# Optimization experiments

Hardware: AMD Instinct MI355X
Metric: run time of the kernel (lower is better)

Reference implementation:

```python
import jax, jax.numpy as jnp
import numpy as np


def setup_inputs() -> dict:
    key = jax.random.key(0)
    z = jax.random.normal(key, (8, 4096, 1024), dtype=jnp.float32)
    return {"z": z}


def reference(z):
    d = z.shape[-1]
    # sort descending along last dim
    z_sorted = -jnp.sort(-z, axis=-1)
    z_cumsum = jnp.cumsum(z_sorted, axis=-1)
    k = jnp.arange(1, d + 1, dtype=z.dtype)  # [d]
    rhs = 1 + k * z_sorted
    is_gt = (rhs > z_cumsum).astype(z.dtype)
    # largest k satisfying the support condition
    k_z = jnp.max(is_gt * k, axis=-1, keepdims=True)  # [..., 1]
    idx = k_z.astype(jnp.int32) - 1
    z_cumsum_k = jnp.take_along_axis(z_cumsum, idx, axis=-1)
    tau = (z_cumsum_k - 1) / k_z
    p = jnp.clip(z - tau, 0.0, None)
    return p
```

## Files before the change

### kernel.cpp

```cpp
#include <hip/hip_runtime.h>


#define ROW_D 1024

typedef float f4 __attribute__((ext_vector_type(4)));

template <int CTRL, int RMASK>
__device__ __forceinline__ float dpp_mv(float x) {
    return __builtin_bit_cast(float, __builtin_amdgcn_update_dpp(
        __builtin_bit_cast(int, x), __builtin_bit_cast(int, x),
        CTRL, RMASK, 0xf, false));
}

__device__ __forceinline__ float dpp_sum_to63(float x) {
    x += dpp_mv<0x111, 0xf>(x);
    x += dpp_mv<0x112, 0xf>(x);
    x += dpp_mv<0x114, 0xf>(x);
    x += dpp_mv<0x118, 0xf>(x);
    x += dpp_mv<0x142, 0xa>(x);
    x += dpp_mv<0x143, 0xc>(x);
    return x;
}
__device__ __forceinline__ float dpp_max_to63(float x) {
    x = fmaxf(x, dpp_mv<0x111, 0xf>(x));
    x = fmaxf(x, dpp_mv<0x112, 0xf>(x));
    x = fmaxf(x, dpp_mv<0x114, 0xf>(x));
    x = fmaxf(x, dpp_mv<0x118, 0xf>(x));
    x = fmaxf(x, dpp_mv<0x142, 0xa>(x));
    x = fmaxf(x, dpp_mv<0x143, 0xc>(x));
    return x;
}
__device__ __forceinline__ float bcast63(float x) {
    return __builtin_bit_cast(float,
        __builtin_amdgcn_readlane(__builtin_bit_cast(int, x), 63));
}

__global__ __launch_bounds__(256) void sparsemax_kernel(
    const float* __restrict__ z, float* __restrict__ out, int nrows) {
    const int lane = (int)(threadIdx.x & 63u);
    const int row  = (int)(blockIdx.x << 2) + (int)(threadIdx.x >> 6);
    if (row >= nrows) return;

    const f4* __restrict__ zin = reinterpret_cast<const f4*>(z + (size_t)row * ROW_D);
    f4* __restrict__ pout      = reinterpret_cast<f4*>(out + (size_t)row * ROW_D);

    f4 v[4];
#pragma unroll
    for (int j = 0; j < 4; ++j) v[j] = zin[lane + 64 * j];

    float mj[4];
#pragma unroll
    for (int j = 0; j < 4; ++j)
        mj[j] = fmaxf(fmaxf(v[j].x, v[j].y), fmaxf(v[j].z, v[j].w));
    float m = fmaxf(fmaxf(mj[0], mj[1]), fmaxf(mj[2], mj[3]));
    m = bcast63(dpp_max_to63(m));

    float t = m - 1.0f;
#pragma unroll 1
    for (int it = 0; it < 16; ++it) {
        float sj[4];
        int n = 0;
#pragma unroll
        for (int j = 0; j < 4; ++j) {
            const float d0 = v[j].x - t, d1 = v[j].y - t;
            const float d2 = v[j].z - t, d3 = v[j].w - t;
            sj[j] = (fmaxf(d0, 0.0f) + fmaxf(d1, 0.0f)) +
                    (fmaxf(d2, 0.0f) + fmaxf(d3, 0.0f));
            n += __popcll(__ballot(d0 > 0.0f));
            n += __popcll(__ballot(d1 > 0.0f));
            n += __popcll(__ballot(d2 > 0.0f));
            n += __popcll(__ballot(d3 > 0.0f));
        }
        float S = bcast63(dpp_sum_to63((sj[0] + sj[1]) + (sj[2] + sj[3])));
        const float t2 = t + (S - 1.0f) / (float)n;
        if (t2 - t <= 1e-6f) { t = t2; break; }
        t = t2;
    }

#pragma unroll
    for (int j = 0; j < 4; ++j) {
        f4 o;
        o.x = fmaxf(v[j].x - t, 0.0f);
        o.y = fmaxf(v[j].y - t, 0.0f);
        o.z = fmaxf(v[j].z - t, 0.0f);
        o.w = fmaxf(v[j].w - t, 0.0f);
        __builtin_nontemporal_store(o, pout + lane + 64 * j);
    }
}

extern "C" void kernel_launch(void* const* d_in, const int* in_sizes, int n_in,
                              void* d_out, int out_size, void* d_ws, size_t ws_size,
                              hipStream_t stream) {
    const float* z = (const float*)d_in[0];
    float* out = (float*)d_out;
    const int n = in_sizes[0];
    const int nrows = n / ROW_D;
    const int blocks = (nrows + 3) / 4;
    sparsemax_kernel<<<blocks, 256, 0, stream>>>(z, out, nrows);
}
```

Measured before the change: 228.5 us.

## Use persistent grid-stride rows with double-buffered row prefetch and fast reciprocal

The kernel becomes persistent: the grid is capped at 2048 blocks and each wave walks rows with a grid stride. While it solves and stores the current row, it prefetches the next row into a second register buffer so load latency overlaps compute. The per-iteration division is replaced by v_rcp_f32, and the loop now exits on the step size. The extra buffer doubles the row registers per lane, which puts pressure on the 8-blocks occupancy hint.

```diff
diff --git a/kernel.cpp b/kernel.cpp
--- a/kernel.cpp
+++ b/kernel.cpp
@@ -34,20 +34,21 @@
     return __builtin_bit_cast(float,
         __builtin_amdgcn_readlane(__builtin_bit_cast(int, x), 63));
 }
+__device__ __forceinline__ float fast_rcp(float x) {
+    float r;
+    asm("v_rcp_f32 %0, %1" : "=v"(r) : "v"(x));
+    return r;
+}
 
-__global__ __launch_bounds__(256) void sparsemax_kernel(
-    const float* __restrict__ z, float* __restrict__ out, int nrows) {
-    const int lane = (int)(threadIdx.x & 63u);
-    const int row  = (int)(blockIdx.x << 2) + (int)(threadIdx.x >> 6);
-    if (row >= nrows) return;
+__device__ __forceinline__ void load_row(f4 (&v)[4], const float* __restrict__ z,
+                                         int row, int lane) {
+    const f4* __restrict__ p = reinterpret_cast<const f4*>(z + (size_t)row * ROW_D);
+#pragma unroll
+    for (int j = 0; j < 4; ++j) v[j] = p[lane + 64 * j];
+}
 
-    const f4* __restrict__ zin = reinterpret_cast<const f4*>(z + (size_t)row * ROW_D);
-    f4* __restrict__ pout      = reinterpret_cast<f4*>(out + (size_t)row * ROW_D);
-
-    f4 v[4];
-#pragma unroll
-    for (int j = 0; j < 4; ++j) v[j] = zin[lane + 64 * j];
-
+__device__ __forceinline__ void solve_store(f4 (&v)[4], float* __restrict__ out,
+                                            int row, int lane) {
     float mj[4];
 #pragma unroll
     for (int j = 0; j < 4; ++j)
@@ -71,12 +72,13 @@
             n += __popcll(__ballot(d2 > 0.0f));
             n += __popcll(__ballot(d3 > 0.0f));
         }
-        float S = bcast63(dpp_sum_to63((sj[0] + sj[1]) + (sj[2] + sj[3])));
-        const float t2 = t + (S - 1.0f) / (float)n;
-        if (t2 - t <= 1e-6f) { t = t2; break; }
-        t = t2;
+        const float S = bcast63(dpp_sum_to63((sj[0] + sj[1]) + (sj[2] + sj[3])));
+        const float step = (S - 1.0f) * fast_rcp((float)n);
+        t += step;
+        if (step <= 1e-6f) break;
     }
 
+    f4* __restrict__ p = reinterpret_cast<f4*>(out + (size_t)row * ROW_D);
 #pragma unroll
     for (int j = 0; j < 4; ++j) {
         f4 o;
@@ -84,7 +86,29 @@
         o.y = fmaxf(v[j].y - t, 0.0f);
         o.z = fmaxf(v[j].z - t, 0.0f);
         o.w = fmaxf(v[j].w - t, 0.0f);
-        __builtin_nontemporal_store(o, pout + lane + 64 * j);
+        __builtin_nontemporal_store(o, p + lane + 64 * j);
+    }
+}
+
+__global__ __launch_bounds__(256, 8) void sparsemax_kernel(
+    const float* __restrict__ z, float* __restrict__ out, int nrows) {
+    const int lane = (int)(threadIdx.x & 63u);
+    int r = (int)(blockIdx.x << 2) + (int)(threadIdx.x >> 6);
+    const int W = (int)(gridDim.x << 2);
+    if (r >= nrows) return;
+
+    f4 A[4], B[4];
+    load_row(A, z, r, lane);
+    int rn = r + W;
+    for (;;) {
+        if (rn < nrows) load_row(B, z, rn, lane);
+        solve_store(A, out, r, lane);
+        if (rn >= nrows) break;
+        r = rn + W;
+        if (r < nrows) load_row(A, z, r, lane);
+        solve_store(B, out, rn, lane);
+        if (r >= nrows) break;
+        rn = r + W;
     }
 }
 
@@ -95,6 +119,8 @@
     float* out = (float*)d_out;
     const int n = in_sizes[0];
     const int nrows = n / ROW_D;
-    const int blocks = (nrows + 3) / 4;
+    int blocks = 2048;
+    const int max_blocks = (nrows + 3) >> 2;
+    if (blocks > max_blocks) blocks = max_blocks;
     sparsemax_kernel<<<blocks, 256, 0, stream>>>(z, out, nrows);
 }
```

Measured after the change: 231.4 us. No clear change (+1.3%).

## Split sparsemax into tau-computation and elementwise apply kernels, use fast reciprocal

Applied to the files above, without the earlier changes.

When workspace is available, the fused kernel is split in two. The first kernel computes the per-row threshold tau and writes it to workspace; a second grid-stride kernel rereads z and writes the clipped output. The Newton step now uses a hardware v_rcp instead of a division, and the fused fallback drops the nontemporal store. The split reads the 128MB input twice to decouple the iterative reduction from the store stream, at the cost of an extra launch and more memory traffic.

```diff
diff --git a/kernel.cpp b/kernel.cpp
--- a/kernel.cpp
+++ b/kernel.cpp
@@ -34,16 +34,19 @@
     return __builtin_bit_cast(float,
         __builtin_amdgcn_readlane(__builtin_bit_cast(int, x), 63));
 }
+__device__ __forceinline__ float fast_rcp(float x) {
+    float r;
+    asm("v_rcp_f32 %0, %1" : "=v"(r) : "v"(x));
+    return r;
+}
 
-__global__ __launch_bounds__(256) void sparsemax_kernel(
-    const float* __restrict__ z, float* __restrict__ out, int nrows) {
+__global__ __launch_bounds__(256) void tau_kernel(
+    const float* __restrict__ z, float* __restrict__ tau, int nrows) {
     const int lane = (int)(threadIdx.x & 63u);
     const int row  = (int)(blockIdx.x << 2) + (int)(threadIdx.x >> 6);
     if (row >= nrows) return;
 
     const f4* __restrict__ zin = reinterpret_cast<const f4*>(z + (size_t)row * ROW_D);
-    f4* __restrict__ pout      = reinterpret_cast<f4*>(out + (size_t)row * ROW_D);
-
     f4 v[4];
 #pragma unroll
     for (int j = 0; j < 4; ++j) v[j] = zin[lane + 64 * j];
@@ -71,12 +74,70 @@
             n += __popcll(__ballot(d2 > 0.0f));
             n += __popcll(__ballot(d3 > 0.0f));
         }
-        float S = bcast63(dpp_sum_to63((sj[0] + sj[1]) + (sj[2] + sj[3])));
-        const float t2 = t + (S - 1.0f) / (float)n;
-        if (t2 - t <= 1e-6f) { t = t2; break; }
-        t = t2;
+        const float S = bcast63(dpp_sum_to63((sj[0] + sj[1]) + (sj[2] + sj[3])));
+        const float step = (S - 1.0f) * fast_rcp((float)n);
+        t += step;
+        if (step <= 1e-6f) break;
     }
+    if (lane == 0) tau[row] = t;
+}
 
+__global__ __launch_bounds__(256) void apply_kernel(
+    const float* __restrict__ z, const float* __restrict__ tau,
+    float* __restrict__ out, int n4) {
+    int i = (int)(blockIdx.x * blockDim.x + threadIdx.x);
+    const int stride = (int)(gridDim.x * blockDim.x);
+    const f4* __restrict__ zi = reinterpret_cast<const f4*>(z);
+    f4* __restrict__ po = reinterpret_cast<f4*>(out);
+    for (; i < n4; i += stride) {
+        const f4 v = zi[i];
+        const float t = tau[i >> 8];
+        f4 o;
+        o.x = fmaxf(v.x - t, 0.0f);
+        o.y = fmaxf(v.y - t, 0.0f);
+        o.z = fmaxf(v.z - t, 0.0f);
+        o.w = fmaxf(v.w - t, 0.0f);
+        po[i] = o;
+    }
+}
+
+__global__ __launch_bounds__(256) void sparsemax_fused(
+    const float* __restrict__ z, float* __restrict__ out, int nrows) {
+    const int lane = (int)(threadIdx.x & 63u);
+    const int row  = (int)(blockIdx.x << 2) + (int)(threadIdx.x >> 6);
+    if (row >= nrows) return;
+    const f4* __restrict__ zin = reinterpret_cast<const f4*>(z + (size_t)row * ROW_D);
+    f4* __restrict__ pout      = reinterpret_cast<f4*>(out + (size_t)row * ROW_D);
+    f4 v[4];
+#pragma unroll
+    for (int j = 0; j < 4; ++j) v[j] = zin[lane + 64 * j];
+    float mj[4];
+#pragma unroll
+    for (int j = 0; j < 4; ++j)
+        mj[j] = fmaxf(fmaxf(v[j].x, v[j].y), fmaxf(v[j].z, v[j].w));
+    float m = fmaxf(fmaxf(mj[0], mj[1]), fmaxf(mj[2], mj[3]));
+    m = bcast63(dpp_max_to63(m));
+    float t = m - 1.0f;
+#pragma unroll 1
+    for (int it = 0; it < 16; ++it) {
+        float sj[4];
+        int n = 0;
+#pragma unroll
+        for (int j = 0; j < 4; ++j) {
+            const float d0 = v[j].x - t, d1 = v[j].y - t;
+            const float d2 = v[j].z - t, d3 = v[j].w - t;
+            sj[j] = (fmaxf(d0, 0.0f) + fmaxf(d1, 0.0f)) +
+                    (fmaxf(d2, 0.0f) + fmaxf(d3, 0.0f));
+            n += __popcll(__ballot(d0 > 0.0f));
+            n += __popcll(__ballot(d1 > 0.0f));
+            n += __popcll(__ballot(d2 > 0.0f));
+            n += __popcll(__ballot(d3 > 0.0f));
+        }
+        const float S = bcast63(dpp_sum_to63((sj[0] + sj[1]) + (sj[2] + sj[3])));
+        const float step = (S - 1.0f) * fast_rcp((float)n);
+        t += step;
+        if (step <= 1e-6f) break;
+    }
 #pragma unroll
     for (int j = 0; j < 4; ++j) {
         f4 o;
@@ -84,7 +145,7 @@
         o.y = fmaxf(v[j].y - t, 0.0f);
         o.z = fmaxf(v[j].z - t, 0.0f);
         o.w = fmaxf(v[j].w - t, 0.0f);
-        __builtin_nontemporal_store(o, pout + lane + 64 * j);
+        pout[lane + 64 * j] = o;
     }
 }
 
@@ -95,6 +156,15 @@
     float* out = (float*)d_out;
     const int n = in_sizes[0];
     const int nrows = n / ROW_D;
-    const int blocks = (nrows + 3) / 4;
-    sparsemax_kernel<<<blocks, 256, 0, stream>>>(z, out, nrows);
+
+    if (d_ws != nullptr && ws_size >= (size_t)nrows * sizeof(float)) {
+        float* tau = (float*)d_ws;
+        const int blocks1 = (nrows + 3) / 4;
+        tau_kernel<<<blocks1, 256, 0, stream>>>(z, tau, nrows);
+        const int n4 = n / 4;
+        apply_kernel<<<2048, 256, 0, stream>>>(z, tau, out, n4);
+    } else {
+        const int blocks = (nrows + 3) / 4;
+        sparsemax_fused<<<blocks, 256, 0, stream>>>(z, out, nrows);
+    }
 }
```

Result: slower. 242.0 us (+5.9%).

## Iterate sparsemax threshold over per-lane top-4 candidates instead of all elements

Applied to the files above, without the earlier changes.

Each lane sorts its 16 values with a small sorting network and keeps the top 4. The Newton iteration for tau then runs only over those candidates whenever no lane's 4th-largest exceeds the starting threshold, with a fallback to the full 16-element loop otherwise. The division is replaced by a hardware reciprocal, and the output store is now a plain store instead of a nontemporal one. This adds sorting-network work up front to cut the per-iteration ALU and ballot cost, at some risk of precision differences from the approximate reciprocal.

```diff
diff --git a/kernel.cpp b/kernel.cpp
--- a/kernel.cpp
+++ b/kernel.cpp
@@ -34,6 +34,34 @@
     return __builtin_bit_cast(float,
         __builtin_amdgcn_readlane(__builtin_bit_cast(int, x), 63));
 }
+__device__ __forceinline__ float fast_rcp(float x) {
+    float r;
+    asm("v_rcp_f32 %0, %1" : "=v"(r) : "v"(x));
+    return r;
+}
+
+__device__ __forceinline__ void ce(float& a, float& b) {
+    const float hi = fmaxf(a, b);
+    const float lo = fminf(a, b);
+    a = hi; b = lo;
+}
+__device__ __forceinline__ void sort4(float& a, float& b, float& c, float& d) {
+    ce(a, b); ce(c, d); ce(a, c); ce(b, d); ce(b, c);
+}
+__device__ __forceinline__ void merge44_top4(
+    float A0, float A1, float A2, float A3,
+    float B0, float B1, float B2, float B3,
+    float& R0, float& R1, float& R2, float& R3) {
+    float e0 = A0, e1 = A2, e2 = B0, e3 = B2;
+    ce(e0, e2); ce(e1, e3); ce(e1, e2);
+    float o0 = A1, o1 = A3, o2 = B1, o3 = B3;
+    ce(o0, o2); ce(o1, o3); ce(o1, o2);
+    R0 = e0;
+    float x = o0, y = e1;
+    ce(x, y);
+    R1 = x; R2 = y;
+    R3 = fmaxf(o1, e2);
+}
 
 __global__ __launch_bounds__(256) void sparsemax_kernel(
     const float* __restrict__ z, float* __restrict__ out, int nrows) {
@@ -48,33 +76,59 @@
 #pragma unroll
     for (int j = 0; j < 4; ++j) v[j] = zin[lane + 64 * j];
 
-    float mj[4];
+    float g[4][4];
 #pragma unroll
-    for (int j = 0; j < 4; ++j)
-        mj[j] = fmaxf(fmaxf(v[j].x, v[j].y), fmaxf(v[j].z, v[j].w));
-    float m = fmaxf(fmaxf(mj[0], mj[1]), fmaxf(mj[2], mj[3]));
-    m = bcast63(dpp_max_to63(m));
+    for (int j = 0; j < 4; ++j) {
+        g[j][0] = v[j].x; g[j][1] = v[j].y; g[j][2] = v[j].z; g[j][3] = v[j].w;
+        sort4(g[j][0], g[j][1], g[j][2], g[j][3]);
+    }
+    float a0, a1, a2, a3, b0, b1, b2, b3, T0, T1, T2, T3;
+    merge44_top4(g[0][0], g[0][1], g[0][2], g[0][3],
+                 g[1][0], g[1][1], g[1][2], g[1][3], a0, a1, a2, a3);
+    merge44_top4(g[2][0], g[2][1], g[2][2], g[2][3],
+                 g[3][0], g[3][1], g[3][2], g[3][3], b0, b1, b2, b3);
+    merge44_top4(a0, a1, a2, a3, b0, b1, b2, b3, T0, T1, T2, T3);
 
+    const float m = bcast63(dpp_max_to63(T0));
     float t = m - 1.0f;
+
+    const unsigned long long bad = __ballot(T3 > t);
+    if (bad == 0ull) {
 #pragma unroll 1
-    for (int it = 0; it < 16; ++it) {
-        float sj[4];
-        int n = 0;
-#pragma unroll
-        for (int j = 0; j < 4; ++j) {
-            const float d0 = v[j].x - t, d1 = v[j].y - t;
-            const float d2 = v[j].z - t, d3 = v[j].w - t;
-            sj[j] = (fmaxf(d0, 0.0f) + fmaxf(d1, 0.0f)) +
-                    (fmaxf(d2, 0.0f) + fmaxf(d3, 0.0f));
-            n += __popcll(__ballot(d0 > 0.0f));
+        for (int it = 0; it < 16; ++it) {
+            const float d0 = T0 - t, d1 = T1 - t, d2 = T2 - t, d3 = T3 - t;
+            const float Sl = (fmaxf(d0, 0.0f) + fmaxf(d1, 0.0f)) +
+                             (fmaxf(d2, 0.0f) + fmaxf(d3, 0.0f));
+            int n = __popcll(__ballot(d0 > 0.0f));
             n += __popcll(__ballot(d1 > 0.0f));
             n += __popcll(__ballot(d2 > 0.0f));
             n += __popcll(__ballot(d3 > 0.0f));
+            const float S = bcast63(dpp_sum_to63(Sl));
+            const float step = (S - 1.0f) * fast_rcp((float)n);
+            t += step;
+            if (step <= 1e-6f) break;
         }
-        float S = bcast63(dpp_sum_to63((sj[0] + sj[1]) + (sj[2] + sj[3])));
-        const float t2 = t + (S - 1.0f) / (float)n;
-        if (t2 - t <= 1e-6f) { t = t2; break; }
-        t = t2;
+    } else {
+#pragma unroll 1
+        for (int it = 0; it < 16; ++it) {
+            float sj[4];
+            int n = 0;
+#pragma unroll
+            for (int j = 0; j < 4; ++j) {
+                const float d0 = v[j].x - t, d1 = v[j].y - t;
+                const float d2 = v[j].z - t, d3 = v[j].w - t;
+                sj[j] = (fmaxf(d0, 0.0f) + fmaxf(d1, 0.0f)) +
+                        (fmaxf(d2, 0.0f) + fmaxf(d3, 0.0f));
+                n += __popcll(__ballot(d0 > 0.0f));
+                n += __popcll(__ballot(d1 > 0.0f));
+                n += __popcll(__ballot(d2 > 0.0f));
+                n += __popcll(__ballot(d3 > 0.0f));
+            }
+            const float S = bcast63(dpp_sum_to63((sj[0] + sj[1]) + (sj[2] + sj[3])));
+            const float step = (S - 1.0f) * fast_rcp((float)n);
+            t += step;
+            if (step <= 1e-6f) break;
+        }
     }
 
 #pragma unroll
@@ -84,7 +138,7 @@
         o.y = fmaxf(v[j].y - t, 0.0f);
         o.z = fmaxf(v[j].z - t, 0.0f);
         o.w = fmaxf(v[j].w - t, 0.0f);
-        __builtin_nontemporal_store(o, pout + lane + 64 * j);
+        pout[lane + 64 * j] = o;
     }
 }
 
```

Result: no change. 226.6 us, median of 2 (-0.8%).
